# Kernel optimization log

Hardware: AMD Instinct MI355X
Metric: run time of the kernel (lower is better)

Reference implementation:

```python
import jax, jax.numpy as jnp
import numpy as np

MIN_NORM = 1e-15
BALL_EPS = 1e-5  # fp32 boundary eps used by hgcn PoincareBall.proj
C_IN = 1.0       # curvature = 1/r_in^2, r_in = 1.0
C_OUT = 1.0      # curvature = 1/r_out^2, r_out = 1.0


def _artanh(x):
    # hgcn clamps to +/-(1-1e-15); use 1e-7 so fp32 does not round to exactly 1
    x = jnp.clip(x, -1.0 + 1e-7, 1.0 - 1e-7)
    return 0.5 * (jnp.log1p(x) - jnp.log1p(-x))


def _norm(x):
    return jnp.maximum(jnp.linalg.norm(x, axis=-1, keepdims=True), MIN_NORM)


def proj(x, c):
    norm = _norm(x)
    maxnorm = (1.0 - BALL_EPS) / jnp.sqrt(c)
    return jnp.where(norm > maxnorm, x / norm * maxnorm, x)


def expmap0(u, c):
    sc = jnp.sqrt(c)
    un = _norm(u)
    return jnp.tanh(sc * un) * u / (sc * un)


def logmap0(p, c):
    sc = jnp.sqrt(c)
    pn = _norm(p)
    return _artanh(sc * pn) * p / (sc * pn)


def mobius_matvec(m, x, c):
    sc = jnp.sqrt(c)
    xn = _norm(x)
    mx = x @ m.T                      # [N, out]
    mxn = _norm(mx)
    res = jnp.tanh(mxn / xn * _artanh(sc * xn)) * mx / (mxn * sc)
    zero_row = jnp.all(mx == 0, axis=-1, keepdims=True)
    return jnp.where(zero_row, jnp.zeros((), dtype=res.dtype), res)


def mobius_add(x, y, c):
    x2 = jnp.sum(x * x, axis=-1, keepdims=True)
    y2 = jnp.sum(y * y, axis=-1, keepdims=True)
    xy = jnp.sum(x * y, axis=-1, keepdims=True)
    num = (1.0 + 2.0 * c * xy + c * y2) * x + (1.0 - c * x2) * y
    denom = 1.0 + 2.0 * c * xy + c * c * x2 * y2
    return num / jnp.maximum(denom, MIN_NORM)


def setup_inputs() -> dict:
    key = jax.random.key(0)
    k1, k2, k3, k4 = jax.random.split(key, 4)
    N, D_IN, D_OUT = 8192, 256, 256
    # points on the ball: small tangent vectors mapped through proj
    x = proj(0.05 * jax.random.normal(k1, (N, D_IN), dtype=jnp.float32), C_IN)
    # dense row-normalized adjacency
    adj = jax.random.uniform(k2, (N, N), dtype=jnp.float32)
    adj = adj / jnp.sum(adj, axis=1, keepdims=True)
    # xavier_uniform with gain sqrt(2)
    bound = np.sqrt(2.0) * np.sqrt(6.0 / (D_IN + D_OUT))
    weight = jax.random.uniform(k3, (D_OUT, D_IN), dtype=jnp.float32,
                                minval=-bound, maxval=bound)
    bias = 0.01 * jax.random.normal(k4, (D_OUT,), dtype=jnp.float32)
    return {"x": x, "adj": adj, "weight": weight, "bias": bias}


def reference(x, adj, weight, bias):
    # --- HypLinear (dropout=0 in eval) ---
    h = proj(mobius_matvec(weight, x, C_IN), C_IN)
    hyp_bias = proj(expmap0(bias[None, :], C_IN), C_IN)  # proj_tan0 = identity
    h = proj(mobius_add(h, hyp_bias, C_IN), C_IN)
    # --- HypAgg (use_att=False): aggregate in tangent space at origin ---
    x_tangent = logmap0(h, C_IN)
    support_t = adj @ x_tangent                          # [N, out]
    h = proj(expmap0(support_t, C_IN), C_IN)
    # --- HypAct: relu in tangent space, re-embed with c_out ---
    xt = jax.nn.relu(logmap0(h, C_IN))                   # proj_tan0 = identity
    return proj(expmap0(xt, C_OUT), C_OUT)
```

## Files before the change

kernel.cpp:

```cpp
#include <hip/hip_runtime.h>
#include <stdint.h>

#define DIM 256
#define NROWS 8192
#define KTOT 8192

typedef unsigned short u16;
typedef short bf16x8 __attribute__((ext_vector_type(8)));
typedef float f32x4 __attribute__((ext_vector_type(4)));

__device__ __forceinline__ u16 f2bf(float x) {
  uint32_t u = __float_as_uint(x);
  u = (u + 0x7FFFu + ((u >> 16) & 1u)) >> 16;
  return (u16)u;
}

__device__ __forceinline__ float wsum(float v) {
  v += __shfl_xor(v, 32, 64);
  v += __shfl_xor(v, 16, 64);
  v += __shfl_xor(v, 8, 64);
  v += __shfl_xor(v, 4, 64);
  v += __shfl_xor(v, 2, 64);
  v += __shfl_xor(v, 1, 64);
  return v;
}

__device__ __forceinline__ float artanh_c(float x) {
  const float lim = 1.0f - 1e-7f;
  x = fminf(fmaxf(x, -lim), lim);
  return 0.5f * (log1pf(x) - log1pf(-x));
}

__global__ __launch_bounds__(256)
void hgcn_k1(const float* __restrict__ x, const float* __restrict__ w,
             float* __restrict__ mx) {
  __shared__ float xs_t[32][64];
  __shared__ float ws_t[32][64];
  int t = threadIdx.x;
  int tx = t & 15, ty = t >> 4;
  int bi = blockIdx.x, bj = blockIdx.y;
  int lr = t >> 2, lc = (t & 3) * 8;
  const float* xp = x + (size_t)(bi * 64 + lr) * DIM + lc;
  const float* wp = w + (size_t)(bj * 64 + lr) * DIM + lc;
  float acc[4][4] = {};
  for (int kb = 0; kb < DIM; kb += 32) {
    float4 a0 = *(const float4*)(xp + kb);
    float4 a1 = *(const float4*)(xp + kb + 4);
    float4 b0 = *(const float4*)(wp + kb);
    float4 b1 = *(const float4*)(wp + kb + 4);
    __syncthreads();
    xs_t[lc + 0][lr] = a0.x; xs_t[lc + 1][lr] = a0.y;
    xs_t[lc + 2][lr] = a0.z; xs_t[lc + 3][lr] = a0.w;
    xs_t[lc + 4][lr] = a1.x; xs_t[lc + 5][lr] = a1.y;
    xs_t[lc + 6][lr] = a1.z; xs_t[lc + 7][lr] = a1.w;
    ws_t[lc + 0][lr] = b0.x; ws_t[lc + 1][lr] = b0.y;
    ws_t[lc + 2][lr] = b0.z; ws_t[lc + 3][lr] = b0.w;
    ws_t[lc + 4][lr] = b1.x; ws_t[lc + 5][lr] = b1.y;
    ws_t[lc + 6][lr] = b1.z; ws_t[lc + 7][lr] = b1.w;
    __syncthreads();
#pragma unroll
    for (int k = 0; k < 32; ++k) {
      float4 xv = *(const float4*)&xs_t[k][ty * 4];
      float4 wv = *(const float4*)&ws_t[k][tx * 4];
      float xr[4] = {xv.x, xv.y, xv.z, xv.w};
      float wr[4] = {wv.x, wv.y, wv.z, wv.w};
#pragma unroll
      for (int ii = 0; ii < 4; ++ii)
#pragma unroll
        for (int jj = 0; jj < 4; ++jj)
          acc[ii][jj] += xr[ii] * wr[jj];
    }
  }
#pragma unroll
  for (int ii = 0; ii < 4; ++ii) {
    float4 o = {acc[ii][0], acc[ii][1], acc[ii][2], acc[ii][3]};
    *(float4*)(mx + (size_t)(bi * 64 + ty * 4 + ii) * DIM + bj * 64 + tx * 4) = o;
  }
}

__global__ __launch_bounds__(256)
void hgcn_k2(const float* __restrict__ x, const float* __restrict__ mx,
             const float* __restrict__ bias, u16* __restrict__ xtT) {
  __shared__ u16 xl[64][256];
  const float maxn = 1.0f - 1e-5f;
  int t = threadIdx.x;
  int wave = t >> 6, lane = t & 63;
  int c0 = lane * 4;

  float4 b4 = *(const float4*)(bias + c0);
  float bn2 = wsum(b4.x * b4.x + b4.y * b4.y + b4.z * b4.z + b4.w * b4.w);
  float bn = fmaxf(sqrtf(bn2), 1e-15f);
  float sb = tanhf(bn) / bn;
  float hbx = b4.x * sb, hby = b4.y * sb, hbz = b4.z * sb, hbw = b4.w * sb;
  float ebn2 = wsum(hbx * hbx + hby * hby + hbz * hbz + hbw * hbw);
  float ebn = fmaxf(sqrtf(ebn2), 1e-15f);
  float sp = ebn > maxn ? maxn / ebn : 1.0f;
  hbx *= sp; hby *= sp; hbz *= sp; hbw *= sp;
  float y2 = (ebn * sp) * (ebn * sp);

  for (int rr = 0; rr < 16; ++rr) {
    int iloc = wave * 16 + rr;
    size_t row = (size_t)blockIdx.x * 64 + iloc;
    float4 xv = *(const float4*)(x + row * DIM + c0);
    float4 mv = *(const float4*)(mx + row * DIM + c0);
    float xn2 = wsum(xv.x * xv.x + xv.y * xv.y + xv.z * xv.z + xv.w * xv.w);
    float mxn2 = wsum(mv.x * mv.x + mv.y * mv.y + mv.z * mv.z + mv.w * mv.w);
    int zloc = (mv.x == 0.0f) && (mv.y == 0.0f) && (mv.z == 0.0f) && (mv.w == 0.0f);
    int zrow = __all(zloc);
    float xn = fmaxf(sqrtf(xn2), 1e-15f);
    float mxn = fmaxf(sqrtf(mxn2), 1e-15f);
    float rfac = tanhf(mxn / xn * artanh_c(xn)) / mxn;
    if (zrow) rfac = 0.0f;
    float hx = mv.x * rfac, hy = mv.y * rfac, hz = mv.z * rfac, hw = mv.w * rfac;
    float hn = fmaxf(fabsf(rfac) * mxn, 1e-15f);
    float s1 = hn > maxn ? maxn / hn : 1.0f;
    hx *= s1; hy *= s1; hz *= s1; hw *= s1;
    float x2 = (hn * s1) * (hn * s1);
    float xy = wsum(hx * hbx + hy * hby + hz * hbz + hw * hbw);
    float ca = 1.0f + 2.0f * xy + y2;
    float cb = 1.0f - x2;
    float den = 1.0f + 2.0f * xy + x2 * y2;
    float inv = 1.0f / fmaxf(den, 1e-15f);
    float ox = (ca * hx + cb * hbx) * inv;
    float oy = (ca * hy + cb * hby) * inv;
    float oz = (ca * hz + cb * hbz) * inv;
    float ow = (ca * hw + cb * hbw) * inv;
    float on2 = wsum(ox * ox + oy * oy + oz * oz + ow * ow);
    float on = fmaxf(sqrtf(on2), 1e-15f);
    float s2 = on > maxn ? maxn / on : 1.0f;
    ox *= s2; oy *= s2; oz *= s2; ow *= s2;
    float pn = fmaxf(on * s2, 1e-15f);
    float lf = artanh_c(pn) / pn;
    u16 tmp[4] = {f2bf(ox * lf), f2bf(oy * lf), f2bf(oz * lf), f2bf(ow * lf)};
    *(uint2*)&xl[iloc][c0] = *(const uint2*)tmp;
  }
  __syncthreads();
  int c = t;
  size_t ob = (size_t)c * KTOT + (size_t)blockIdx.x * 64;
  for (int ch = 0; ch < 8; ++ch) {
    u16 tmp[8];
#pragma unroll
    for (int q = 0; q < 8; ++q) tmp[q] = xl[ch * 8 + q][c];
    *(uint4*)(xtT + ob + ch * 8) = *(const uint4*)tmp;
  }
}

#define A_TILE (256 * 64)
#define B_TILE (64 * 64)

__device__ __forceinline__ void k3_issueA(const u16* __restrict__ xtT, u16* __restrict__ dstbase,
                                          int kabs, int wave, int lane) {
#pragma unroll
  for (int q = 0; q < 4; ++q) {
    int sb = (q * 8 + wave) * 64;
    int slot = sb + lane;
    int n = slot >> 3;
    int sch = (slot & 7) ^ (n & 7);
    __builtin_amdgcn_global_load_lds(
        (const __attribute__((address_space(1))) void*)(xtT + (size_t)n * KTOT + kabs + sch * 8),
        (__attribute__((address_space(3))) void*)(dstbase + sb * 8), 16, 0, 0);
  }
}

__device__ __forceinline__ void k3_writeB(u16* __restrict__ bbuf, int rowB, int chB,
                                          const float4& ra, const float4& rb) {
  u16 tmp[8] = {f2bf(ra.x), f2bf(ra.y), f2bf(ra.z), f2bf(ra.w),
                f2bf(rb.x), f2bf(rb.y), f2bf(rb.z), f2bf(rb.w)};
  *(uint4*)&bbuf[rowB * 64 + (chB ^ (rowB & 7)) * 8] = *(const uint4*)tmp;
}

__device__ __forceinline__ void k3_compute(const u16* __restrict__ ba, const u16* __restrict__ bb,
                                           f32x4 (&acc)[4][2], int wm, int wn, int l15, int l4) {
  __builtin_amdgcn_s_setprio(1);
#pragma unroll
  for (int kc = 0; kc < 2; ++kc) {
    bf16x8 bfr[2];
#pragma unroll
    for (int mi = 0; mi < 2; ++mi) {
      int r = wm * 32 + mi * 16 + l15;
      int ch = (kc * 4 + l4) ^ (r & 7);
      bfr[mi] = *(const bf16x8*)&bb[r * 64 + ch * 8];
    }
#pragma unroll
    for (int ni = 0; ni < 4; ++ni) {
      int rn = wn * 64 + ni * 16 + l15;
      int ch = (kc * 4 + l4) ^ (rn & 7);
      bf16x8 afr = *(const bf16x8*)&ba[rn * 64 + ch * 8];
      acc[ni][0] = __builtin_amdgcn_mfma_f32_16x16x32_bf16(afr, bfr[0], acc[ni][0], 0, 0, 0);
      acc[ni][1] = __builtin_amdgcn_mfma_f32_16x16x32_bf16(afr, bfr[1], acc[ni][1], 0, 0, 0);
    }
  }
  __builtin_amdgcn_s_setprio(0);
}

#define K3_WAITV(N) { asm volatile("s_waitcnt vmcnt(" #N ")" ::: "memory"); __builtin_amdgcn_sched_barrier(0); }
#define K3_LGKM0    { asm volatile("s_waitcnt lgkmcnt(0)" ::: "memory"); __builtin_amdgcn_sched_barrier(0); }

#define K3_BODY(S, RCA, RCB, RIA, RIB, DOISSUE)                                        \
  {                                                                                    \
    K3_WAITV(4);             \
    k3_writeB(ldsB + (((S) + 1) % 3) * B_TILE, rowB, chB, RCA, RCB);                   \
    K3_LGKM0;                                                                          \
    __builtin_amdgcn_s_barrier();                  \
    if (DOISSUE) {                                                                     \
      const float* ap = adjp + ((S) + 2) * 64;                                         \
      RIA = *(const float4*)ap;                                                        \
      RIB = *(const float4*)(ap + 4);                                                  \
      __builtin_amdgcn_sched_barrier(0);                                               \
      k3_issueA(xtT, ldsA + (((S) + 2) % 3) * A_TILE, kbase + ((S) + 2) * 64, wave, lane); \
      __builtin_amdgcn_sched_barrier(0);                                               \
    }                                                                                  \
    k3_compute(ldsA + ((S) % 3) * A_TILE, ldsB + ((S) % 3) * B_TILE, acc, wm, wn, l15, l4); \
  }

__global__ __launch_bounds__(512, 2)
void hgcn_k3(const float* __restrict__ adj, const u16* __restrict__ xtT,
             float* __restrict__ p0, float* __restrict__ p1) {
  __shared__ u16 ldsA[3 * A_TILE];
  __shared__ u16 ldsB[3 * B_TILE];
  int t = threadIdx.x;
  int wave = t >> 6, lane = t & 63;
  int l15 = lane & 15, l4 = lane >> 4;
  int wm = wave >> 2, wn = wave & 3;

  int bid = blockIdx.x;
  int xcd = bid & 7;
  int y = xcd >> 2;
  int m_tile = (bid >> 3) * 4 + (xcd & 3);
  int m0 = m_tile * 64;
  int kbase = y * (KTOT / 2);
  float* outp = y ? p1 : p0;

  int rowB = t >> 3, chB = t & 7;
  const float* adjp = adj + (size_t)(m0 + rowB) * KTOT + kbase + chB * 8;

  f32x4 acc[4][2];
#pragma unroll
  for (int i = 0; i < 4; ++i)
#pragma unroll
    for (int j = 0; j < 2; ++j)
      acc[i][j] = (f32x4){0.f, 0.f, 0.f, 0.f};

  float4 r0a, r0b, r1a, r1b;
  r0a = *(const float4*)adjp;
  r0b = *(const float4*)(adjp + 4);
  __builtin_amdgcn_sched_barrier(0);
  k3_issueA(xtT, ldsA, kbase, wave, lane);
  __builtin_amdgcn_sched_barrier(0);
  r1a = *(const float4*)(adjp + 64);
  r1b = *(const float4*)(adjp + 64 + 4);
  __builtin_amdgcn_sched_barrier(0);
  k3_issueA(xtT, ldsA + A_TILE, kbase + 64, wave, lane);
  __builtin_amdgcn_sched_barrier(0);
  K3_WAITV(10);
  k3_writeB(ldsB, rowB, chB, r0a, r0b);

  for (int s = 0; s < 62; s += 2) {
    K3_BODY(s, r1a, r1b, r0a, r0b, true);
    K3_BODY(s + 1, r0a, r0b, r1a, r1b, true);
  }
  K3_BODY(62, r1a, r1b, r0a, r0b, false);
  K3_WAITV(0);
  __builtin_amdgcn_s_barrier();
  k3_compute(ldsA + (63 % 3) * A_TILE, ldsB + (63 % 3) * B_TILE, acc, wm, wn, l15, l4);

#pragma unroll
  for (int ni = 0; ni < 4; ++ni)
#pragma unroll
    for (int mi = 0; mi < 2; ++mi) {
      int n = wn * 64 + ni * 16 + l4 * 4;
      int m = m0 + wm * 32 + mi * 16 + l15;
      *(f32x4*)(outp + (size_t)m * DIM + n) = acc[ni][mi];
    }
}

__global__ __launch_bounds__(256)
void hgcn_k4(const float* __restrict__ p0, const float* __restrict__ p1,
             float* __restrict__ out) {
  const float maxn = 1.0f - 1e-5f;
  int t = threadIdx.x;
  int wave = t >> 6, lane = t & 63;
  size_t row = (size_t)blockIdx.x * 4 + wave;
  int c0 = lane * 4;
  float4 a = *(const float4*)(p0 + row * DIM + c0);
  float4 b = *(const float4*)(p1 + row * DIM + c0);
  float sx = a.x + b.x, sy = a.y + b.y, sz = a.z + b.z, sw = a.w + b.w;
  float un2 = wsum(sx * sx + sy * sy + sz * sz + sw * sw);
  float un = fmaxf(sqrtf(un2), 1e-15f);
  float t1 = tanhf(un) / un;
  float hx = sx * t1, hy = sy * t1, hz = sz * t1, hw = sw * t1;
  float hn = fmaxf(fabsf(t1) * un, 1e-15f);
  float s1 = hn > maxn ? maxn / hn : 1.0f;
  hx *= s1; hy *= s1; hz *= s1; hw *= s1;
  float pn = fmaxf(hn * s1, 1e-15f);
  float lf = artanh_c(pn) / pn;
  float rx = fmaxf(hx * lf, 0.0f), ry = fmaxf(hy * lf, 0.0f);
  float rz = fmaxf(hz * lf, 0.0f), rw = fmaxf(hw * lf, 0.0f);
  float rn2 = wsum(rx * rx + ry * ry + rz * rz + rw * rw);
  float rn = fmaxf(sqrtf(rn2), 1e-15f);
  float t2 = tanhf(rn) / rn;
  float ox = rx * t2, oy = ry * t2, oz = rz * t2, ow = rw * t2;
  float on = fmaxf(fabsf(t2) * rn, 1e-15f);
  float s3 = on > maxn ? maxn / on : 1.0f;
  float4 o = {ox * s3, oy * s3, oz * s3, ow * s3};
  *(float4*)(out + row * DIM + c0) = o;
}

extern "C" void kernel_launch(void* const* d_in, const int* in_sizes, int n_in,
                              void* d_out, int out_size, void* d_ws, size_t ws_size,
                              hipStream_t stream) {
  const float* x = (const float*)d_in[0];
  const float* adj = (const float*)d_in[1];
  const float* wgt = (const float*)d_in[2];
  const float* bias = (const float*)d_in[3];
  float* out = (float*)d_out;
  char* ws = (char*)d_ws;
  float* mx = (float*)ws;
  u16* xtT = (u16*)(ws + (8u << 20));
  float* p1 = (float*)(ws + (12u << 20));
  float* p0 = mx;

  hipLaunchKernelGGL(hgcn_k1, dim3(128, 4), dim3(256), 0, stream, x, wgt, mx);
  hipLaunchKernelGGL(hgcn_k2, dim3(128), dim3(256), 0, stream, x, mx, bias, xtT);
  hipLaunchKernelGGL(hgcn_k3, dim3(256), dim3(512), 0, stream, adj, xtT, p0, p1);
  hipLaunchKernelGGL(hgcn_k4, dim3(2048), dim3(256), 0, stream, p0, p1, out);
}
```

Measured before the change: 172.8 us.

## Enlarge adjacency GEMM M tile to 128 rows and add four-way K split

The aggregation GEMM block now covers 128 adjacency rows instead of 64, and each thread loads 16 adj floats per step. This halves how often each xtT tile is re-read per row of output and raises the MFMA-to-load ratio. When the workspace is large enough, K is split four ways, with two extra partial buffers that the epilogue sums, so the grid size stays the same. The cost is lower occupancy (one block per CU), more accumulator registers, larger LDS use, and extra partial-sum traffic.

Result: faster. 158.6 us (-8.2%).

```diff
diff --git a/kernel.cpp b/kernel.cpp
--- a/kernel.cpp
+++ b/kernel.cpp
@@ -146,7 +146,9 @@
 }
 
 #define A_TILE (256 * 64)
-#define B_TILE (64 * 64)
+#define B_TILE (128 * 64)
+
+struct Bq { float4 a, b, c, d; };
 
 __device__ __forceinline__ void k3_issueA(const u16* __restrict__ xtT, u16* __restrict__ dstbase,
                                           int kabs, int wave, int lane) {
@@ -162,22 +164,26 @@
   }
 }
 
-__device__ __forceinline__ void k3_writeB(u16* __restrict__ bbuf, int rowB, int chB,
-                                          const float4& ra, const float4& rb) {
-  u16 tmp[8] = {f2bf(ra.x), f2bf(ra.y), f2bf(ra.z), f2bf(ra.w),
-                f2bf(rb.x), f2bf(rb.y), f2bf(rb.z), f2bf(rb.w)};
-  *(uint4*)&bbuf[rowB * 64 + (chB ^ (rowB & 7)) * 8] = *(const uint4*)tmp;
+__device__ __forceinline__ void k3_writeB(u16* __restrict__ bbuf, int rowB, int cq, const Bq& r) {
+  u16 tmp[16] = {f2bf(r.a.x), f2bf(r.a.y), f2bf(r.a.z), f2bf(r.a.w),
+                 f2bf(r.b.x), f2bf(r.b.y), f2bf(r.b.z), f2bf(r.b.w),
+                 f2bf(r.c.x), f2bf(r.c.y), f2bf(r.c.z), f2bf(r.c.w),
+                 f2bf(r.d.x), f2bf(r.d.y), f2bf(r.d.z), f2bf(r.d.w)};
+  int c0 = (2 * cq) ^ (rowB & 7);
+  int c1 = (2 * cq + 1) ^ (rowB & 7);
+  *(uint4*)&bbuf[rowB * 64 + c0 * 8] = ((const uint4*)tmp)[0];
+  *(uint4*)&bbuf[rowB * 64 + c1 * 8] = ((const uint4*)tmp)[1];
 }
 
 __device__ __forceinline__ void k3_compute(const u16* __restrict__ ba, const u16* __restrict__ bb,
-                                           f32x4 (&acc)[4][2], int wm, int wn, int l15, int l4) {
+                                           f32x4 (&acc)[4][4], int wm, int wn, int l15, int l4) {
   __builtin_amdgcn_s_setprio(1);
 #pragma unroll
   for (int kc = 0; kc < 2; ++kc) {
-    bf16x8 bfr[2];
-#pragma unroll
-    for (int mi = 0; mi < 2; ++mi) {
-      int r = wm * 32 + mi * 16 + l15;
+    bf16x8 bfr[4];
+#pragma unroll
+    for (int mi = 0; mi < 4; ++mi) {
+      int r = wm * 64 + mi * 16 + l15;
       int ch = (kc * 4 + l4) ^ (r & 7);
       bfr[mi] = *(const bf16x8*)&bb[r * 64 + ch * 8];
     }
@@ -186,8 +192,9 @@
       int rn = wn * 64 + ni * 16 + l15;
       int ch = (kc * 4 + l4) ^ (rn & 7);
       bf16x8 afr = *(const bf16x8*)&ba[rn * 64 + ch * 8];
-      acc[ni][0] = __builtin_amdgcn_mfma_f32_16x16x32_bf16(afr, bfr[0], acc[ni][0], 0, 0, 0);
-      acc[ni][1] = __builtin_amdgcn_mfma_f32_16x16x32_bf16(afr, bfr[1], acc[ni][1], 0, 0, 0);
+#pragma unroll
+      for (int mi = 0; mi < 4; ++mi)
+        acc[ni][mi] = __builtin_amdgcn_mfma_f32_16x16x32_bf16(afr, bfr[mi], acc[ni][mi], 0, 0, 0);
     }
   }
   __builtin_amdgcn_s_setprio(0);
@@ -196,16 +203,16 @@
 #define K3_WAITV(N) { asm volatile("s_waitcnt vmcnt(" #N ")" ::: "memory"); __builtin_amdgcn_sched_barrier(0); }
 #define K3_LGKM0    { asm volatile("s_waitcnt lgkmcnt(0)" ::: "memory"); __builtin_amdgcn_sched_barrier(0); }
 
-#define K3_BODY(S, RCA, RCB, RIA, RIB, DOISSUE)                                        \
+#define K3_BODY(S, RC, RI, DOISSUE)                                                    \
   {                                                                                    \
-    K3_WAITV(4);             \
-    k3_writeB(ldsB + (((S) + 1) % 3) * B_TILE, rowB, chB, RCA, RCB);                   \
+    K3_WAITV(4);                                                                       \
+    k3_writeB(ldsB + (((S) + 1) % 3) * B_TILE, rowB, cq, RC);                          \
     K3_LGKM0;                                                                          \
-    __builtin_amdgcn_s_barrier();                  \
+    __builtin_amdgcn_s_barrier();                                                      \
     if (DOISSUE) {                                                                     \
       const float* ap = adjp + ((S) + 2) * 64;                                         \
-      RIA = *(const float4*)ap;                                                        \
-      RIB = *(const float4*)(ap + 4);                                                  \
+      RI.a = ((const float4*)ap)[0]; RI.b = ((const float4*)ap)[1];                    \
+      RI.c = ((const float4*)ap)[2]; RI.d = ((const float4*)ap)[3];                    \
       __builtin_amdgcn_sched_barrier(0);                                               \
       k3_issueA(xtT, ldsA + (((S) + 2) % 3) * A_TILE, kbase + ((S) + 2) * 64, wave, lane); \
       __builtin_amdgcn_sched_barrier(0);                                               \
@@ -213,9 +220,11 @@
     k3_compute(ldsA + ((S) % 3) * A_TILE, ldsB + ((S) % 3) * B_TILE, acc, wm, wn, l15, l4); \
   }
 
-__global__ __launch_bounds__(512, 2)
+__global__ __launch_bounds__(512, 1)
 void hgcn_k3(const float* __restrict__ adj, const u16* __restrict__ xtT,
-             float* __restrict__ p0, float* __restrict__ p1) {
+             float* __restrict__ p0, float* __restrict__ p1,
+             float* __restrict__ p2, float* __restrict__ p3,
+             int xps_log, int ksize) {
   __shared__ u16 ldsA[3 * A_TILE];
   __shared__ u16 ldsB[3 * B_TILE];
   int t = threadIdx.x;
@@ -224,67 +233,80 @@
   int wm = wave >> 2, wn = wave & 3;
 
   int bid = blockIdx.x;
-  int xcd = bid & 7;
-  int y = xcd >> 2;
-  int m_tile = (bid >> 3) * 4 + (xcd & 3);
-  int m0 = m_tile * 64;
-  int kbase = y * (KTOT / 2);
-  float* outp = y ? p1 : p0;
-
-  int rowB = t >> 3, chB = t & 7;
-  const float* adjp = adj + (size_t)(m0 + rowB) * KTOT + kbase + chB * 8;
-
-  f32x4 acc[4][2];
+  int xps = 1 << xps_log;
+  int split = (bid & 7) >> xps_log;
+  int sub = (bid & 7) & (xps - 1);
+  int m_tile = (bid >> 3) * xps + sub;
+  int m0 = m_tile * 128;
+  int kbase = split * ksize;
+  float* outp = split == 0 ? p0 : split == 1 ? p1 : split == 2 ? p2 : p3;
+  const int NSTEP = ksize >> 6;
+
+  int rowB = t >> 2, cq = t & 3;
+  const float* adjp = adj + (size_t)(m0 + rowB) * KTOT + kbase + cq * 16;
+
+  f32x4 acc[4][4];
 #pragma unroll
   for (int i = 0; i < 4; ++i)
 #pragma unroll
-    for (int j = 0; j < 2; ++j)
+    for (int j = 0; j < 4; ++j)
       acc[i][j] = (f32x4){0.f, 0.f, 0.f, 0.f};
 
-  float4 r0a, r0b, r1a, r1b;
-  r0a = *(const float4*)adjp;
-  r0b = *(const float4*)(adjp + 4);
+  Bq rA, rB;
+  rA.a = ((const float4*)adjp)[0]; rA.b = ((const float4*)adjp)[1];
+  rA.c = ((const float4*)adjp)[2]; rA.d = ((const float4*)adjp)[3];
   __builtin_amdgcn_sched_barrier(0);
   k3_issueA(xtT, ldsA, kbase, wave, lane);
   __builtin_amdgcn_sched_barrier(0);
-  r1a = *(const float4*)(adjp + 64);
-  r1b = *(const float4*)(adjp + 64 + 4);
+  {
+    const float* ap = adjp + 64;
+    rB.a = ((const float4*)ap)[0]; rB.b = ((const float4*)ap)[1];
+    rB.c = ((const float4*)ap)[2]; rB.d = ((const float4*)ap)[3];
+  }
   __builtin_amdgcn_sched_barrier(0);
   k3_issueA(xtT, ldsA + A_TILE, kbase + 64, wave, lane);
   __builtin_amdgcn_sched_barrier(0);
-  K3_WAITV(10);
-  k3_writeB(ldsB, rowB, chB, r0a, r0b);
-
-  for (int s = 0; s < 62; s += 2) {
-    K3_BODY(s, r1a, r1b, r0a, r0b, true);
-    K3_BODY(s + 1, r0a, r0b, r1a, r1b, true);
-  }
-  K3_BODY(62, r1a, r1b, r0a, r0b, false);
+  K3_WAITV(12);
+  k3_writeB(ldsB, rowB, cq, rA);
+
+  for (int s = 0; s < NSTEP - 2; s += 2) {
+    K3_BODY(s, rB, rA, true);
+    K3_BODY(s + 1, rA, rB, true);
+  }
+  K3_BODY(NSTEP - 2, rB, rA, false);
   K3_WAITV(0);
   __builtin_amdgcn_s_barrier();
-  k3_compute(ldsA + (63 % 3) * A_TILE, ldsB + (63 % 3) * B_TILE, acc, wm, wn, l15, l4);
+  k3_compute(ldsA + ((NSTEP - 1) % 3) * A_TILE, ldsB + ((NSTEP - 1) % 3) * B_TILE,
+             acc, wm, wn, l15, l4);
 
 #pragma unroll
   for (int ni = 0; ni < 4; ++ni)
 #pragma unroll
-    for (int mi = 0; mi < 2; ++mi) {
+    for (int mi = 0; mi < 4; ++mi) {
       int n = wn * 64 + ni * 16 + l4 * 4;
-      int m = m0 + wm * 32 + mi * 16 + l15;
+      int m = m0 + wm * 64 + mi * 16 + l15;
       *(f32x4*)(outp + (size_t)m * DIM + n) = acc[ni][mi];
     }
 }
 
 __global__ __launch_bounds__(256)
 void hgcn_k4(const float* __restrict__ p0, const float* __restrict__ p1,
-             float* __restrict__ out) {
+             const float* __restrict__ p2, const float* __restrict__ p3,
+             int nsplit, float* __restrict__ out) {
   const float maxn = 1.0f - 1e-5f;
   int t = threadIdx.x;
   int wave = t >> 6, lane = t & 63;
   size_t row = (size_t)blockIdx.x * 4 + wave;
   int c0 = lane * 4;
-  float4 a = *(const float4*)(p0 + row * DIM + c0);
-  float4 b = *(const float4*)(p1 + row * DIM + c0);
+  size_t off = row * DIM + c0;
+  float4 a = *(const float4*)(p0 + off);
+  float4 b = *(const float4*)(p1 + off);
   float sx = a.x + b.x, sy = a.y + b.y, sz = a.z + b.z, sw = a.w + b.w;
+  if (nsplit == 4) {
+    float4 c = *(const float4*)(p2 + off);
+    float4 d = *(const float4*)(p3 + off);
+    sx += c.x + d.x; sy += c.y + d.y; sz += c.z + d.z; sw += c.w + d.w;
+  }
   float un2 = wsum(sx * sx + sy * sy + sz * sz + sw * sw);
   float un = fmaxf(sqrtf(un2), 1e-15f);
   float t1 = tanhf(un) / un;
@@ -303,7 +325,7 @@
   float on = fmaxf(fabsf(t2) * rn, 1e-15f);
   float s3 = on > maxn ? maxn / on : 1.0f;
   float4 o = {ox * s3, oy * s3, oz * s3, ow * s3};
-  *(float4*)(out + row * DIM + c0) = o;
+  *(float4*)(out + off) = o;
 }
 
 extern "C" void kernel_launch(void* const* d_in, const int* in_sizes, int n_in,
@@ -318,10 +340,18 @@
   float* mx = (float*)ws;
   u16* xtT = (u16*)(ws + (8u << 20));
   float* p1 = (float*)(ws + (12u << 20));
+  float* p2 = (float*)(ws + (20u << 20));
+  float* p3 = (float*)(ws + (28u << 20));
   float* p0 = mx;
+
+  int nsplit = (ws_size >= ((size_t)36 << 20)) ? 4 : 2;
+  int xps_log = (nsplit == 4) ? 1 : 2;
+  int ksize = KTOT / nsplit;
+  if (nsplit == 2) { p2 = p0; p3 = p0; }
 
   hipLaunchKernelGGL(hgcn_k1, dim3(128, 4), dim3(256), 0, stream, x, wgt, mx);
   hipLaunchKernelGGL(hgcn_k2, dim3(128), dim3(256), 0, stream, x, mx, bias, xtT);
-  hipLaunchKernelGGL(hgcn_k3, dim3(256), dim3(512), 0, stream, adj, xtT, p0, p1);
-  hipLaunchKernelGGL(hgcn_k4, dim3(2048), dim3(256), 0, stream, p0, p1, out);
-}
+  hipLaunchKernelGGL(hgcn_k3, dim3(64 * nsplit), dim3(512), 0, stream,
+                     adj, xtT, p0, p1, p2, p3, xps_log, ksize);
+  hipLaunchKernelGGL(hgcn_k4, dim3(2048), dim3(256), 0, stream, p0, p1, p2, p3, nsplit, out);
+}
```
